# Performance work log

Hardware: AMD Instinct MI355X
Metric: run time of the kernel (lower is better)

The kernel has to match this reference:

```python
import jax, jax.numpy as jnp
import numpy as np

TOKENS, D_IN, D_OUT = 8192, 4096, 4096

def setup_inputs() -> dict:
    key = jax.random.key(0)
    k1, k2, k3 = jax.random.split(key, 3)
    x = jax.random.normal(k1, (TOKENS, D_IN), dtype=jnp.float32)
    # original init: uniform(-1, 1) on weights of shape [out, in]
    w_pos = jax.random.uniform(k2, (D_OUT, D_IN), dtype=jnp.float32, minval=-1.0, maxval=1.0)
    w_neg = jax.random.uniform(k3, (D_OUT, D_IN), dtype=jnp.float32, minval=-1.0, maxval=1.0)
    return {"x": x, "w_pos": w_pos, "w_neg": w_neg}

def _ste_binarize(w):
    # (w > 0).float() in fwd, identity grad (STE): stop_grad(bin - w) + w
    b = (w > 0).astype(w.dtype)
    return jax.lax.stop_gradient(b - w) + w

def reference(x, w_pos, w_neg):
    tern_pos = _ste_binarize(w_pos)  # [O, I]
    tern_neg = _ste_binarize(w_neg)  # [O, I]
    # y = x @ tern_pos^T - x @ tern_neg^T  (biases unused in original forward)
    y = jnp.einsum('ti,oi->to', x, tern_pos) - jnp.einsum('ti,oi->to', x, tern_neg)
    return y
```

## Files before the change

kernel.cpp:

```cpp
#include <hip/hip_runtime.h>
#include <hip/hip_cooperative_groups.h>
#include <stdint.h>

namespace cg = cooperative_groups;


#define TOKENS 8192
#define DIN    4096
#define DOUT   4096

typedef __bf16  bf16x8  __attribute__((ext_vector_type(8)));
typedef float   floatx4 __attribute__((ext_vector_type(4)));
typedef float   f32x4   __attribute__((ext_vector_type(4)));
typedef unsigned short u16x4 __attribute__((ext_vector_type(4)));

__device__ __forceinline__ void async_copy16(const void* g, void* l) {
  __builtin_amdgcn_global_load_lds(
      (const __attribute__((address_space(1))) void*)g,
      (__attribute__((address_space(3))) void*)l, 16, 0, 0);
}

__device__ __forceinline__ unsigned short f2bf_rne(float f) {
  union { float f; uint32_t u; } v; v.f = f;
  uint32_t u = v.u;
  u += 0x7fffu + ((u >> 16) & 1u);
  return (unsigned short)(u >> 16);
}

__device__ __forceinline__ unsigned short tern_bits(float p, float n) {
  bool bp = p > 0.0f, bn = n > 0.0f;
  return (unsigned short)(bp == bn ? 0u : (bp ? 0x3f80u : 0xbf80u));
}


#define LDS_BUF   65536u
#define LDS_B_OFF 32768u
#define LDS_KC    16384u

__global__ __launch_bounds__(512, 2) void fused_kernel(
    const float* __restrict__ x,
    const float* __restrict__ wp,
    const float* __restrict__ wn,
    unsigned short* __restrict__ xb,
    unsigned short* __restrict__ tern,
    float* __restrict__ C)
{
  __shared__ __align__(16) char lds[131072];

  const int tid = threadIdx.x;
  const uint32_t b = blockIdx.x;

  {
    const f32x4* xf = (const f32x4*)x;
    u16x4* xo = (u16x4*)xb;
    uint32_t i = b * 32768u + (uint32_t)tid;
#pragma unroll 4
    for (int j = 0; j < 64; ++j, i += 512u) {
      f32x4 v = __builtin_nontemporal_load(&xf[i]);
      u16x4 o;
      o.x = f2bf_rne(v.x); o.y = f2bf_rne(v.y);
      o.z = f2bf_rne(v.z); o.w = f2bf_rne(v.w);
      xo[i] = o;
    }
    const f32x4* wpf = (const f32x4*)wp;
    const f32x4* wnf = (const f32x4*)wn;
    u16x4* to = (u16x4*)tern;
    uint32_t k = b * 16384u + (uint32_t)tid;
#pragma unroll 4
    for (int j = 0; j < 32; ++j, k += 512u) {
      f32x4 p = __builtin_nontemporal_load(&wpf[k]);
      f32x4 n = __builtin_nontemporal_load(&wnf[k]);
      u16x4 o;
      o.x = tern_bits(p.x, n.x);
      o.y = tern_bits(p.y, n.y);
      o.z = tern_bits(p.z, n.z);
      o.w = tern_bits(p.w, n.w);
      to[k] = o;
    }
  }

  asm volatile("s_waitcnt vmcnt(0) lgkmcnt(0)" ::: "memory");
  cg::this_grid().sync();
  __builtin_amdgcn_sched_barrier(0);

  const int lane  = tid & 63;
  const int wid   = tid >> 6;
  const int waveM = wid >> 2;
  const int waveN = wid & 3;

  const int mrow = lane & 15;
  const int q    = lane >> 4;
  const int xs   = (q ^ ((mrow >> 1) & 3)) * 16;
  const uint32_t ldsBase =
      (uint32_t)(uintptr_t)(__attribute__((address_space(3))) char*)lds;
  const uint32_t aFragBase = (uint32_t)waveM * 8192u + (uint32_t)mrow * 64u + (uint32_t)xs;
  const uint32_t bFragBase = LDS_B_OFF + (uint32_t)waveN * 4096u
                           + (uint32_t)mrow * 64u + (uint32_t)xs;
  const uint32_t aA0 = ldsBase + aFragBase;
  const uint32_t aA1 = aA0 + LDS_BUF;
  const uint32_t bA0 = ldsBase + bFragBase;
  const uint32_t bA1 = bA0 + LDS_BUF;

  const uint32_t srow  = (uint32_t)wid * 32u + (uint32_t)(lane >> 2);
  const uint32_t slot  = (uint32_t)(tid & 3);
  const uint32_t chnk  = slot ^ ((srow >> 1) & 3u);
  const uint32_t ldsSt = (uint32_t)(tid >> 6) * 2048u
                       + (uint32_t)(tid & 63) * 16u;
  const char* Ab = (const char*)xb;
  const char* Bb = (const char*)tern;

  floatx4 a0f[4], a1f[4], b0f[4], b1f[4];
  floatx4 acc[8][4];

#define DSR(DST, ADDR, IMM)                                                \
  asm volatile("ds_read_b128 %0, %1 offset:%c2"                            \
               : "=v"(DST) : "v"(ADDR), "i"(IMM))

#define IA4(DST, ADDR, KC, MH) do {                                        \
    DSR(DST[0], ADDR, (KC) * 16384 + ((MH) * 4 + 0) * 1024);               \
    DSR(DST[1], ADDR, (KC) * 16384 + ((MH) * 4 + 1) * 1024);               \
    DSR(DST[2], ADDR, (KC) * 16384 + ((MH) * 4 + 2) * 1024);               \
    DSR(DST[3], ADDR, (KC) * 16384 + ((MH) * 4 + 3) * 1024);               \
  } while (0)

#define IB2(DST, N0, ADDR, KC) do {                                        \
    DSR(DST[N0],     ADDR, (KC) * 16384 + ((N0)) * 1024);                  \
    DSR(DST[N0 + 1], ADDR, (KC) * 16384 + ((N0) + 1) * 1024);              \
  } while (0)

#define STAGE_A(BUF, KH, KB) do {                                          \
    uint32_t g_ = stA + (KB) + (KH) * 64u;                                 \
    uint32_t l_ = (BUF) * LDS_BUF + (KH) * LDS_KC + ldsSt;                 \
    async_copy16(Ab + g_,           lds + l_);                             \
    async_copy16(Ab + g_ + 131072u, lds + l_ + 1024u);                     \
  } while (0)

#define STAGE_B(BUF, KH, KB) do {                                          \
    uint32_t g_ = stB + (KB) + (KH) * 64u;                                 \
    uint32_t l_ = (BUF) * LDS_BUF + LDS_B_OFF + (KH) * LDS_KC + ldsSt;     \
    async_copy16(Bb + g_,           lds + l_);                             \
    async_copy16(Bb + g_ + 131072u, lds + l_ + 1024u);                     \
  } while (0)

#define PHASE(MH, AF, BF, ISSUE_STMT, STAGE_STMT) do {                     \
    asm volatile("s_waitcnt lgkmcnt(0)" ::: "memory");                     \
    asm volatile("s_waitcnt vmcnt(8)" ::: "memory");                       \
    __builtin_amdgcn_sched_barrier(0);                                     \
    ISSUE_STMT;                                                            \
    __builtin_amdgcn_sched_barrier(0);                                     \
    __builtin_amdgcn_s_setprio(1);                                         \
    _Pragma("unroll")                                                      \
    for (int m_ = 0; m_ < 4; ++m_)                                         \
      _Pragma("unroll")                                                    \
      for (int n_ = 0; n_ < 4; ++n_)                                       \
        acc[(MH) * 4 + m_][n_] = __builtin_amdgcn_mfma_f32_16x16x32_bf16(  \
            __builtin_bit_cast(bf16x8, AF[m_]),                            \
            __builtin_bit_cast(bf16x8, BF[n_]),                            \
            acc[(MH) * 4 + m_][n_], 0, 0, 0);                              \
    __builtin_amdgcn_s_setprio(0);                                         \
    STAGE_STMT;                                                            \
    __builtin_amdgcn_s_barrier();                                          \
  } while (0)

#pragma unroll 1
  for (int t = 0; t < 2; ++t) {
    const uint32_t flat = b + (uint32_t)t * 256u;
    const uint32_t swz  = ((flat & 7u) << 6) | (flat >> 3);
    const uint32_t bm = (swz >> 4) * 256u;
    const uint32_t bn = (swz & 15u) * 256u;
    const uint32_t stA = (bm + srow) * (DIN * 2u) + chnk * 16u;
    const uint32_t stB = (bn + srow) * (DIN * 2u) + chnk * 16u;

#pragma unroll
    for (int m = 0; m < 8; ++m)
#pragma unroll
      for (int n = 0; n < 4; ++n)
        acc[m][n] = (floatx4)0.0f;

    asm volatile("s_waitcnt lgkmcnt(0)" ::: "memory");
    asm volatile("s_waitcnt vmcnt(0)" ::: "memory");
    __builtin_amdgcn_s_barrier();

    STAGE_B(0, 0, 0u);
    STAGE_A(0, 0, 0u);
    STAGE_B(0, 1, 0u);
    STAGE_A(0, 1, 0u);
    STAGE_B(1, 0, 128u);
    STAGE_A(1, 0, 128u);
    STAGE_B(1, 1, 128u);
    asm volatile("s_waitcnt vmcnt(8)" ::: "memory");
    __builtin_amdgcn_s_barrier();
    IB2(b0f, 0, bA0, 0); IB2(b0f, 2, bA0, 0);
    IA4(a0f, aA0, 0, 0);

#pragma unroll 1
    for (int i = 0; i < 32; ++i) {
      const uint32_t kb1 = (uint32_t)(2 * i + 1) * 128u;
      const uint32_t kb2 = (uint32_t)((2 * i + 2) & 63) * 128u;
      const uint32_t kb3 = (uint32_t)((2 * i + 3) & 63) * 128u;

      PHASE(0, a0f, b0f, { IA4(a1f, aA0, 0, 1); IB2(b1f, 0, bA0, 1); },
            STAGE_A(1, 1, kb1));
      PHASE(1, a1f, b0f, { IA4(a0f, aA0, 1, 0); IB2(b1f, 2, bA0, 1); },
            STAGE_B(0, 0, kb2));
      PHASE(0, a0f, b1f, { IA4(a1f, aA0, 1, 1); IB2(b0f, 0, bA1, 0); },
            STAGE_A(0, 0, kb2));
      PHASE(1, a1f, b1f, { IA4(a0f, aA1, 0, 0); IB2(b0f, 2, bA1, 0); },
            STAGE_B(0, 1, kb2));
      PHASE(0, a0f, b0f, { IA4(a1f, aA1, 0, 1); IB2(b1f, 0, bA1, 1); },
            STAGE_A(0, 1, kb2));
      PHASE(1, a1f, b0f, { IA4(a0f, aA1, 1, 0); IB2(b1f, 2, bA1, 1); },
            STAGE_B(1, 0, kb3));
      PHASE(0, a0f, b1f, { IA4(a1f, aA1, 1, 1); IB2(b0f, 0, bA0, 0); },
            STAGE_A(1, 0, kb3));
      PHASE(1, a1f, b1f, { IA4(a0f, aA0, 0, 0); IB2(b0f, 2, bA0, 0); },
            STAGE_B(1, 1, kb3));
    }

    const int col0 = (int)bn + waveN * 64 + (lane & 15);
    const int row0 = (int)bm + waveM * 128 + (lane >> 4) * 4;
    float* Cp = C + (size_t)row0 * DOUT + col0;
#pragma unroll
    for (int m = 0; m < 8; ++m)
#pragma unroll
      for (int n = 0; n < 4; ++n)
#pragma unroll
        for (int r = 0; r < 4; ++r)
          Cp[(size_t)(m * 16 + r) * DOUT + n * 16] = acc[m][n][r];
  }

#undef DSR
#undef IA4
#undef IB2
#undef STAGE_A
#undef STAGE_B
#undef PHASE
}

extern "C" void kernel_launch(void* const* d_in, const int* in_sizes, int n_in,
                              void* d_out, int out_size, void* d_ws, size_t ws_size,
                              hipStream_t stream) {
  const float* x  = (const float*)d_in[0];
  const float* wp = (const float*)d_in[1];
  const float* wn = (const float*)d_in[2];
  float* out = (float*)d_out;

  unsigned short* xb   = (unsigned short*)d_ws;
  unsigned short* tern = xb + (size_t)TOKENS * DIN;

  void* args[6] = {
      (void*)&x, (void*)&wp, (void*)&wn,
      (void*)&xb, (void*)&tern, (void*)&out,
  };
  (void)hipLaunchCooperativeKernel((const void*)fused_kernel,
                                   dim3(256), dim3(512), args, 0, stream);
}
```

Measured before the change: 528.5 us.

## Switch GEMM main loop from 16x16x32 to 32x32x16 bf16 MFMA

Replaces the 16x16x32 MFMA tiling with 32x32x16 MFMA: each wave now computes 4x2 32x32 accumulator tiles instead of 8x4 16x16 tiles. LDS fragment addressing, the XOR swizzle for global-to-LDS staging and the epilogue store mapping are reworked to match the new fragment layout, with even/odd k-halves selected by an address XOR. The aim is fewer MFMA and LDS read instructions per FLOP and higher matrix-core throughput. The risk is that the new swizzle adds LDS bank conflicts or that the layout change introduces indexing errors.

```diff
diff --git a/kernel.cpp b/kernel.cpp
--- a/kernel.cpp
+++ b/kernel.cpp
@@ -9,9 +9,10 @@
 #define DIN    4096
 #define DOUT   4096
 
-typedef __bf16  bf16x8  __attribute__((ext_vector_type(8)));
-typedef float   floatx4 __attribute__((ext_vector_type(4)));
-typedef float   f32x4   __attribute__((ext_vector_type(4)));
+typedef __bf16  bf16x8   __attribute__((ext_vector_type(8)));
+typedef float   floatx4  __attribute__((ext_vector_type(4)));
+typedef float   floatx16 __attribute__((ext_vector_type(16)));
+typedef float   f32x4    __attribute__((ext_vector_type(4)));
 typedef unsigned short u16x4 __attribute__((ext_vector_type(4)));
 
 __device__ __forceinline__ void async_copy16(const void* g, void* l) {
@@ -45,7 +46,7 @@
     unsigned short* __restrict__ tern,
     float* __restrict__ C)
 {
-  __shared__ __align__(16) char lds[131072];
+  __shared__ __align__(128) char lds[131072];
 
   const int tid = threadIdx.x;
   const uint32_t b = blockIdx.x;
@@ -88,61 +89,64 @@
   const int waveM = wid >> 2;
   const int waveN = wid & 3;
 
-  const int mrow = lane & 15;
-  const int q    = lane >> 4;
-  const int xs   = (q ^ ((mrow >> 1) & 3)) * 16;
+  const int r5 = lane & 31;
+  const int q  = lane >> 5;
+  const uint32_t fr = (((uint32_t)r5 >> 1) ^ ((uint32_t)r5 >> 3)) & 3u;
   const uint32_t ldsBase =
       (uint32_t)(uintptr_t)(__attribute__((address_space(3))) char*)lds;
-  const uint32_t aFragBase = (uint32_t)waveM * 8192u + (uint32_t)mrow * 64u + (uint32_t)xs;
-  const uint32_t bFragBase = LDS_B_OFF + (uint32_t)waveN * 4096u
-                           + (uint32_t)mrow * 64u + (uint32_t)xs;
-  const uint32_t aA0 = ldsBase + aFragBase;
-  const uint32_t aA1 = aA0 + LDS_BUF;
-  const uint32_t bA0 = ldsBase + bFragBase;
-  const uint32_t bA1 = bA0 + LDS_BUF;
+  const uint32_t slotA = ((uint32_t)q ^ fr) * 16u;
+  const uint32_t aE0 = ldsBase + (uint32_t)waveM * 8192u
+                     + (uint32_t)r5 * 64u + slotA;
+  const uint32_t aO0 = aE0 ^ 32u;
+  const uint32_t aE1 = aE0 + LDS_BUF;
+  const uint32_t aO1 = aO0 + LDS_BUF;
+  const uint32_t bE0 = ldsBase + LDS_B_OFF + (uint32_t)waveN * 4096u
+                     + (uint32_t)r5 * 64u + slotA;
+  const uint32_t bO0 = bE0 ^ 32u;
+  const uint32_t bE1 = bE0 + LDS_BUF;
+  const uint32_t bO1 = bO0 + LDS_BUF;
 
   const uint32_t srow  = (uint32_t)wid * 32u + (uint32_t)(lane >> 2);
   const uint32_t slot  = (uint32_t)(tid & 3);
-  const uint32_t chnk  = slot ^ ((srow >> 1) & 3u);
-  const uint32_t ldsSt = (uint32_t)(tid >> 6) * 2048u
-                       + (uint32_t)(tid & 63) * 16u;
+  const uint32_t chnk  = slot ^ ((((srow >> 1) ^ (srow >> 3))) & 3u);
+  const uint32_t ldsSt = (uint32_t)wid * 2048u + (uint32_t)lane * 16u;
   const char* Ab = (const char*)xb;
   const char* Bb = (const char*)tern;
 
-  floatx4 a0f[4], a1f[4], b0f[4], b1f[4];
-  floatx4 acc[8][4];
+  floatx4 a0f[4], a1f[4], b0f[2], b1f[2];
+  floatx16 acc[4][2];
 
 #define DSR(DST, ADDR, IMM)                                                \
   asm volatile("ds_read_b128 %0, %1 offset:%c2"                            \
                : "=v"(DST) : "v"(ADDR), "i"(IMM))
 
-#define IA4(DST, ADDR, KC, MH) do {                                        \
-    DSR(DST[0], ADDR, (KC) * 16384 + ((MH) * 4 + 0) * 1024);               \
-    DSR(DST[1], ADDR, (KC) * 16384 + ((MH) * 4 + 1) * 1024);               \
-    DSR(DST[2], ADDR, (KC) * 16384 + ((MH) * 4 + 2) * 1024);               \
-    DSR(DST[3], ADDR, (KC) * 16384 + ((MH) * 4 + 3) * 1024);               \
-  } while (0)
-
-#define IB2(DST, N0, ADDR, KC) do {                                        \
-    DSR(DST[N0],     ADDR, (KC) * 16384 + ((N0)) * 1024);                  \
-    DSR(DST[N0 + 1], ADDR, (KC) * 16384 + ((N0) + 1) * 1024);              \
+#define IA4(DST, ADDR, KC2) do {                                           \
+    DSR(DST[0], ADDR, (KC2) * 16384 + 0 * 2048);                           \
+    DSR(DST[1], ADDR, (KC2) * 16384 + 1 * 2048);                           \
+    DSR(DST[2], ADDR, (KC2) * 16384 + 2 * 2048);                           \
+    DSR(DST[3], ADDR, (KC2) * 16384 + 3 * 2048);                           \
+  } while (0)
+
+#define IB2(DST, ADDR, KC2) do {                                           \
+    DSR(DST[0], ADDR, (KC2) * 16384 + 0 * 2048);                           \
+    DSR(DST[1], ADDR, (KC2) * 16384 + 1 * 2048);                           \
   } while (0)
 
 #define STAGE_A(BUF, KH, KB) do {                                          \
     uint32_t g_ = stA + (KB) + (KH) * 64u;                                 \
     uint32_t l_ = (BUF) * LDS_BUF + (KH) * LDS_KC + ldsSt;                 \
-    async_copy16(Ab + g_,           lds + l_);                             \
-    async_copy16(Ab + g_ + 131072u, lds + l_ + 1024u);                     \
+    async_copy16(Ab + g_,                     lds + l_);                   \
+    async_copy16(Ab + ((g_ ^ 32u) + 131072u), lds + l_ + 1024u);           \
   } while (0)
 
 #define STAGE_B(BUF, KH, KB) do {                                          \
     uint32_t g_ = stB + (KB) + (KH) * 64u;                                 \
     uint32_t l_ = (BUF) * LDS_BUF + LDS_B_OFF + (KH) * LDS_KC + ldsSt;     \
-    async_copy16(Bb + g_,           lds + l_);                             \
-    async_copy16(Bb + g_ + 131072u, lds + l_ + 1024u);                     \
-  } while (0)
-
-#define PHASE(MH, AF, BF, ISSUE_STMT, STAGE_STMT) do {                     \
+    async_copy16(Bb + g_,                     lds + l_);                   \
+    async_copy16(Bb + ((g_ ^ 32u) + 131072u), lds + l_ + 1024u);           \
+  } while (0)
+
+#define PHASE(AF, BF, ISSUE_STMT, STAGE_STMT) do {                         \
     asm volatile("s_waitcnt lgkmcnt(0)" ::: "memory");                     \
     asm volatile("s_waitcnt vmcnt(8)" ::: "memory");                       \
     __builtin_amdgcn_sched_barrier(0);                                     \
@@ -152,11 +156,11 @@
     _Pragma("unroll")                                                      \
     for (int m_ = 0; m_ < 4; ++m_)                                         \
       _Pragma("unroll")                                                    \
-      for (int n_ = 0; n_ < 4; ++n_)                                       \
-        acc[(MH) * 4 + m_][n_] = __builtin_amdgcn_mfma_f32_16x16x32_bf16(  \
+      for (int n_ = 0; n_ < 2; ++n_)                                       \
+        acc[m_][n_] = __builtin_amdgcn_mfma_f32_32x32x16_bf16(             \
             __builtin_bit_cast(bf16x8, AF[m_]),                            \
             __builtin_bit_cast(bf16x8, BF[n_]),                            \
-            acc[(MH) * 4 + m_][n_], 0, 0, 0);                              \
+            acc[m_][n_], 0, 0, 0);                                         \
     __builtin_amdgcn_s_setprio(0);                                         \
     STAGE_STMT;                                                            \
     __builtin_amdgcn_s_barrier();                                          \
@@ -172,10 +176,10 @@
     const uint32_t stB = (bn + srow) * (DIN * 2u) + chnk * 16u;
 
 #pragma unroll
-    for (int m = 0; m < 8; ++m)
-#pragma unroll
-      for (int n = 0; n < 4; ++n)
-        acc[m][n] = (floatx4)0.0f;
+    for (int m = 0; m < 4; ++m)
+#pragma unroll
+      for (int n = 0; n < 2; ++n)
+        acc[m][n] = (floatx16)0.0f;
 
     asm volatile("s_waitcnt lgkmcnt(0)" ::: "memory");
     asm volatile("s_waitcnt vmcnt(0)" ::: "memory");
@@ -190,8 +194,8 @@
     STAGE_B(1, 1, 128u);
     asm volatile("s_waitcnt vmcnt(8)" ::: "memory");
     __builtin_amdgcn_s_barrier();
-    IB2(b0f, 0, bA0, 0); IB2(b0f, 2, bA0, 0);
-    IA4(a0f, aA0, 0, 0);
+    IA4(a0f, aE0, 0);
+    IB2(b0f, bE0, 0);
 
 #pragma unroll 1
     for (int i = 0; i < 32; ++i) {
@@ -199,34 +203,37 @@
       const uint32_t kb2 = (uint32_t)((2 * i + 2) & 63) * 128u;
       const uint32_t kb3 = (uint32_t)((2 * i + 3) & 63) * 128u;
 
-      PHASE(0, a0f, b0f, { IA4(a1f, aA0, 0, 1); IB2(b1f, 0, bA0, 1); },
+      PHASE(a0f, b0f, { IA4(a1f, aO0, 0); IB2(b1f, bO0, 0); },
             STAGE_A(1, 1, kb1));
-      PHASE(1, a1f, b0f, { IA4(a0f, aA0, 1, 0); IB2(b1f, 2, bA0, 1); },
+      PHASE(a1f, b1f, { IA4(a0f, aE0, 1); IB2(b0f, bE0, 1); },
             STAGE_B(0, 0, kb2));
-      PHASE(0, a0f, b1f, { IA4(a1f, aA0, 1, 1); IB2(b0f, 0, bA1, 0); },
+      PHASE(a0f, b0f, { IA4(a1f, aO0, 1); IB2(b1f, bO0, 1); },
             STAGE_A(0, 0, kb2));
-      PHASE(1, a1f, b1f, { IA4(a0f, aA1, 0, 0); IB2(b0f, 2, bA1, 0); },
+      PHASE(a1f, b1f, { IA4(a0f, aE1, 0); IB2(b0f, bE1, 0); },
             STAGE_B(0, 1, kb2));
-      PHASE(0, a0f, b0f, { IA4(a1f, aA1, 0, 1); IB2(b1f, 0, bA1, 1); },
+      PHASE(a0f, b0f, { IA4(a1f, aO1, 0); IB2(b1f, bO1, 0); },
             STAGE_A(0, 1, kb2));
-      PHASE(1, a1f, b0f, { IA4(a0f, aA1, 1, 0); IB2(b1f, 2, bA1, 1); },
+      PHASE(a1f, b1f, { IA4(a0f, aE1, 1); IB2(b0f, bE1, 1); },
             STAGE_B(1, 0, kb3));
-      PHASE(0, a0f, b1f, { IA4(a1f, aA1, 1, 1); IB2(b0f, 0, bA0, 0); },
+      PHASE(a0f, b0f, { IA4(a1f, aO1, 1); IB2(b1f, bO1, 1); },
             STAGE_A(1, 0, kb3));
-      PHASE(1, a1f, b1f, { IA4(a0f, aA0, 0, 0); IB2(b0f, 2, bA0, 0); },
+      PHASE(a1f, b1f, { IA4(a0f, aE0, 0); IB2(b0f, bE0, 0); },
             STAGE_B(1, 1, kb3));
     }
 
-    const int col0 = (int)bn + waveN * 64 + (lane & 15);
-    const int row0 = (int)bm + waveM * 128 + (lane >> 4) * 4;
+    const int col0 = (int)bn + waveN * 64 + r5;
+    const int row0 = (int)bm + waveM * 128 + q * 4;
     float* Cp = C + (size_t)row0 * DOUT + col0;
 #pragma unroll
-    for (int m = 0; m < 8; ++m)
-#pragma unroll
-      for (int n = 0; n < 4; ++n)
-#pragma unroll
-        for (int r = 0; r < 4; ++r)
-          Cp[(size_t)(m * 16 + r) * DOUT + n * 16] = acc[m][n][r];
+    for (int m = 0; m < 4; ++m)
+#pragma unroll
+      for (int n = 0; n < 2; ++n)
+#pragma unroll
+        for (int g = 0; g < 4; ++g)
+#pragma unroll
+          for (int e = 0; e < 4; ++e)
+            Cp[(size_t)(m * 32 + g * 8 + e) * DOUT + n * 32] =
+                acc[m][n][g * 4 + e];
   }
 
 #undef DSR
```

Result: slower. 549.2 us (+3.9%).
